# Optimization experiments

Hardware: AMD Instinct MI355X
Metric: run time of the kernel (lower is better)

Reference implementation:

```python
import jax, jax.numpy as jnp
import numpy as np

KSIZE = 5

def _sigmas(ksize, sigma_color, sigma_space):
    if sigma_space == 0:
        sigma_space = 0.15 * ksize + 0.35
    if sigma_color == 0:
        sigma_color = sigma_space
    return sigma_color, sigma_space

def _space_kernel(ksize, sigma):
    # matches getGaussianKernel (sigma > 0 branch)
    xs = jnp.arange(ksize, dtype=jnp.float32) - ksize // 2
    k1 = jnp.exp(-xs**2 / (2.0 * sigma * sigma))
    k2 = k1[:, None] * k1[None, :]
    return k2 / k2.sum()

def bilateral(x, ksize, sigma_color, sigma_space):
    sigma_color, sigma_space = _sigmas(ksize, sigma_color, sigma_space)
    pad = (ksize - 1) // 2
    B, C, H, W = x.shape
    xp = jnp.pad(x, ((0, 0), (0, 0), (pad, pad), (pad, pad)), mode='reflect')
    # patches[b,c,h,w,ki,kj] == padded[b,c,h+ki,w+kj] (same layout as torch unfold)
    patches = jnp.stack(
        [xp[:, :, i:i + H, j:j + W] for i in range(ksize) for j in range(ksize)],
        axis=-1,
    ).reshape(B, C, H, W, ksize, ksize)
    diff = patches - x[..., None, None]
    w_color = jnp.exp(-diff**2 / (2.0 * sigma_color * sigma_color))
    w_color = w_color / w_color.sum(axis=(-1, -2), keepdims=True)
    w_space = _space_kernel(ksize, sigma_space)  # [k,k], broadcasts
    w = w_color * w_space
    return (w * patches).sum(axis=(-1, -2)) / w.sum(axis=(-1, -2))

def setup_inputs() -> dict:
    key = jax.random.key(0)
    x = jax.random.uniform(key, (16, 3, 512, 512), dtype=jnp.float32)
    return {"x": x}

def reference(x):
    return bilateral(x, KSIZE, 0.0, 0.0)
```

## Files before the change

kernel.cpp:

```cpp
#include <hip/hip_runtime.h>


constexpr int H_ = 512;
constexpr int W_ = 512;

__global__ __launch_bounds__(256, 3) void bilateral_kernel(
    const float* __restrict__ x,
    float* __restrict__ out,
    int nthreads)
{
    int t = blockIdx.x * 256 + threadIdx.x;
    if (t >= nthreads) return;

    int qx = t & 127;
    int rg = (t >> 7) & 127;
    int pl = t >> 14;
    int w0 = qx << 2;
    int h0 = rg << 2;
    const float* plane = x + ((long)pl << 18);
    float* oplane = out + ((long)pl << 18);

    int aL = max(w0 - 2, 0);
    int aR = min(w0 + 4, W_ - 2);
    bool bL = (w0 == 0);
    bool bR = (w0 == W_ - 4);

    float Wn[8][8];
#pragma unroll
    for (int k = 0; k < 8; ++k) {
        int r = h0 + k - 2;
        r = min(abs(r), 2 * (H_ - 1) - r);
        const float* rp = plane + r * W_;
        float2 l2 = *(const float2*)(rp + aL);
        float4 c4 = *(const float4*)(rp + w0);
        float2 r2 = *(const float2*)(rp + aR);
        Wn[k][2] = c4.x; Wn[k][3] = c4.y; Wn[k][4] = c4.z; Wn[k][5] = c4.w;
        Wn[k][0] = bL ? c4.z : l2.x;
        Wn[k][1] = l2.y;
        Wn[k][6] = r2.x;
        Wn[k][7] = bR ? c4.y : r2.y;
    }

    const float coef2 = -0.59615498f;

#pragma unroll
    for (int oi = 0; oi < 4; ++oi) {
        float num[4] = {0.f, 0.f, 0.f, 0.f};
        float den[4] = {0.f, 0.f, 0.f, 0.f};
#pragma unroll
        for (int q = 0; q < 4; ++q) {
            float c = Wn[oi + 2][q + 2];
#pragma unroll
            for (int di = 0; di < 5; ++di) {
#pragma unroll
                for (int dj = 0; dj < 5; ++dj) {
                    float p = Wn[oi + di][q + dj];
                    float cs = coef2 * (float)((di - 2) * (di - 2) +
                                               (dj - 2) * (dj - 2));
                    float d = p - c;
                    float e = d * coef2;
                    float arg = fmaf(e, d, cs);
                    float w = __builtin_amdgcn_exp2f(arg);
                    num[q] = fmaf(w, p, num[q]);
                    den[q] += w;
                }
            }
        }
        float4 o;
        o.x = num[0] * __builtin_amdgcn_rcpf(den[0]);
        o.y = num[1] * __builtin_amdgcn_rcpf(den[1]);
        o.z = num[2] * __builtin_amdgcn_rcpf(den[2]);
        o.w = num[3] * __builtin_amdgcn_rcpf(den[3]);
        *(float4*)(oplane + (h0 + oi) * W_ + w0) = o;
    }
}

extern "C" void kernel_launch(void* const* d_in, const int* in_sizes, int n_in,
                              void* d_out, int out_size, void* d_ws, size_t ws_size,
                              hipStream_t stream)
{
    const float* x = (const float*)d_in[0];
    float* out = (float*)d_out;
    int nthreads = in_sizes[0] >> 4;
    int blocks = (nthreads + 255) / 256;
    bilateral_kernel<<<blocks, 256, 0, stream>>>(x, out, nthreads);
}
```

Baseline: 137.2 us.

## Exploit weight symmetry to share exp computations across pixels in the thread tile

Restructures the per-thread 4x4 output computation to iterate over half of the neighbour offsets and reuse each pairwise weight for both pixels when both lie inside the tile. The center contribution is folded in as an initial value. This removes roughly a quarter of the exp2 evaluations and difference computations. All 32 accumulators stay live at once, which raises register pressure under the existing launch bounds. An empty asm barrier pins the loaded window in registers.

```diff
diff --git a/kernel.cpp b/kernel.cpp
--- a/kernel.cpp
+++ b/kernel.cpp
@@ -41,37 +41,73 @@
         Wn[k][7] = bR ? c4.y : r2.y;
     }
 
+#pragma unroll
+    for (int k = 0; k < 8; ++k)
+#pragma unroll
+        for (int j = 0; j < 8; ++j)
+            asm volatile("" : "+v"(Wn[k][j]));
+    __builtin_amdgcn_sched_barrier(0);
+
     const float coef2 = -0.59615498f;
 
+    float num[4][4], den[4][4];
 #pragma unroll
-    for (int oi = 0; oi < 4; ++oi) {
-        float num[4] = {0.f, 0.f, 0.f, 0.f};
-        float den[4] = {0.f, 0.f, 0.f, 0.f};
+    for (int ai = 0; ai < 4; ++ai)
 #pragma unroll
-        for (int q = 0; q < 4; ++q) {
-            float c = Wn[oi + 2][q + 2];
+        for (int aj = 0; aj < 4; ++aj) {
+            num[ai][aj] = Wn[ai + 2][aj + 2];
+            den[ai][aj] = 1.0f;
+        }
+
 #pragma unroll
-            for (int di = 0; di < 5; ++di) {
+    for (int di = 0; di <= 2; ++di) {
 #pragma unroll
-                for (int dj = 0; dj < 5; ++dj) {
-                    float p = Wn[oi + di][q + dj];
-                    float cs = coef2 * (float)((di - 2) * (di - 2) +
-                                               (dj - 2) * (dj - 2));
-                    float d = p - c;
-                    float e = d * coef2;
-                    float arg = fmaf(e, d, cs);
-                    float w = __builtin_amdgcn_exp2f(arg);
-                    num[q] = fmaf(w, p, num[q]);
-                    den[q] += w;
+        for (int dj = -2; dj <= 2; ++dj) {
+            if (di == 0 && dj <= 0) continue;
+            const float cs = coef2 * (float)(di * di + dj * dj);
+
+#pragma unroll
+            for (int ai = 0; ai < 4; ++ai) {
+#pragma unroll
+                for (int aj = 0; aj < 4; ++aj) {
+                    float pa = Wn[ai + 2][aj + 2];
+                    float pb = Wn[ai + 2 + di][aj + 2 + dj];
+                    float d = pb - pa;
+                    float w = __builtin_amdgcn_exp2f(fmaf(d * coef2, d, cs));
+                    num[ai][aj] = fmaf(w, pb, num[ai][aj]);
+                    den[ai][aj] += w;
+                    if (ai + di <= 3 && aj + dj >= 0 && aj + dj <= 3) {
+                        num[ai + di][aj + dj] =
+                            fmaf(w, pa, num[ai + di][aj + dj]);
+                        den[ai + di][aj + dj] += w;
+                    }
+                }
+            }
+#pragma unroll
+            for (int ai = 0; ai < 4; ++ai) {
+#pragma unroll
+                for (int aj = 0; aj < 4; ++aj) {
+                    if (ai - di >= 0 && aj - dj >= 0 && aj - dj <= 3)
+                        continue;
+                    float pa = Wn[ai + 2][aj + 2];
+                    float pb = Wn[ai + 2 - di][aj + 2 - dj];
+                    float d = pb - pa;
+                    float w = __builtin_amdgcn_exp2f(fmaf(d * coef2, d, cs));
+                    num[ai][aj] = fmaf(w, pb, num[ai][aj]);
+                    den[ai][aj] += w;
                 }
             }
         }
+    }
+
+#pragma unroll
+    for (int ai = 0; ai < 4; ++ai) {
         float4 o;
-        o.x = num[0] * __builtin_amdgcn_rcpf(den[0]);
-        o.y = num[1] * __builtin_amdgcn_rcpf(den[1]);
-        o.z = num[2] * __builtin_amdgcn_rcpf(den[2]);
-        o.w = num[3] * __builtin_amdgcn_rcpf(den[3]);
-        *(float4*)(oplane + (h0 + oi) * W_ + w0) = o;
+        o.x = num[ai][0] * __builtin_amdgcn_rcpf(den[ai][0]);
+        o.y = num[ai][1] * __builtin_amdgcn_rcpf(den[ai][1]);
+        o.z = num[ai][2] * __builtin_amdgcn_rcpf(den[ai][2]);
+        o.w = num[ai][3] * __builtin_amdgcn_rcpf(den[ai][3]);
+        *(float4*)(oplane + (h0 + ai) * W_ + w0) = o;
     }
 }
 
```

After: 152.0 us. +10.8%, slower.
